# Kernel tuning notes

Measured on AMD Instinct MI355X. Metric: run time of the kernel, lower is better.

Reference implementation:

```python
import jax, jax.numpy as jnp
import numpy as np

D_MODEL = 2048
EXP_RATE = 4
DEPTH = 1
EPS = 1e-5

def setup_inputs() -> dict:
    key = jax.random.key(0)
    k1, k2 = jax.random.split(key, 2)
    B, T, D, E = 4, 4096, D_MODEL, EXP_RATE
    x = jax.random.normal(k1, (B, T, D), dtype=jnp.float32)
    residual = jax.random.normal(k2, (B, T, D), dtype=jnp.float32)
    # static_alpha = cat([alpha0, eye(E)], dim=1) -> [E, E+1]
    alpha0 = np.zeros((E, 1), dtype=np.float32)
    alpha0[DEPTH % E, 0] = 1.0
    static_alpha = jnp.asarray(np.concatenate([alpha0, np.eye(E, dtype=np.float32)], axis=1))
    static_beta = jnp.ones((E,), dtype=jnp.float32)
    dynamic_alpha_fn = jnp.zeros((D, E + 1), dtype=jnp.float32)
    dynamic_alpha_scale = jnp.ones((1,), dtype=jnp.float32) * 0.01
    dynamic_beta_fn = jnp.zeros((D,), dtype=jnp.float32)
    dynamic_beta_scale = jnp.ones((1,), dtype=jnp.float32) * 0.01
    rms_weight = jnp.ones((D,), dtype=jnp.float32)
    return {
        "x": x, "residual": residual, "rms_weight": rms_weight,
        "static_alpha": static_alpha, "static_beta": static_beta,
        "dynamic_alpha_fn": dynamic_alpha_fn, "dynamic_alpha_scale": dynamic_alpha_scale,
        "dynamic_beta_fn": dynamic_beta_fn, "dynamic_beta_scale": dynamic_beta_scale,
    }

def reference(x, residual, rms_weight, static_alpha, static_beta,
              dynamic_alpha_fn, dynamic_alpha_scale, dynamic_beta_fn, dynamic_beta_scale):
    # RMSNorm (elementwise affine)
    norm_x = x * jax.lax.rsqrt(jnp.mean(x * x, axis=-1, keepdims=True) + EPS) * rms_weight
    # Dynamic params
    dyn_alpha = jnp.tanh(norm_x @ dynamic_alpha_fn) * dynamic_alpha_scale  # [B,T,E+1]
    dyn_beta = jnp.tanh(norm_x @ dynamic_beta_fn) * dynamic_beta_scale[0]  # [B,T]
    alpha = static_alpha[None, None] + dyn_alpha[:, :, None, :]  # [B,T,E,E+1]
    beta = static_beta[None, None] + dyn_beta[:, :, None]        # [B,T,E]
    # Width connection: einsum('btij,btjd->btid', alpha^T, x_expanded) with
    # x_expanded[b,t,j,:] == x[b,t,:] for all j  =>  mix_h[b,t,i,:] = (sum_j alpha[b,t,j,i]) * x[b,t,:]
    coeff = alpha.sum(axis=2)  # [B,T,E+1]
    # Depth connection: sum_e beta_e * residual + sum_{i>=1} mix_h_i  (dropout = identity at eval)
    out = residual * beta.sum(axis=-1, keepdims=True) + x * coeff[..., 1:].sum(axis=-1, keepdims=True)
    return out
```

## Files before the change

### kernel.cpp

```cpp
#include <hip/hip_runtime.h>


#define D_MODEL 2048
#define E_RATE 4
#define HC_EPS 1e-5f
#define NT 256
#define EPT 8
#define TPB 8

__device__ __forceinline__ float fast_tanh(float z) {
    const float e = __builtin_amdgcn_exp2f(z * 2.8853900817779268f);
    return fmaf(-2.0f, __builtin_amdgcn_rcpf(e + 1.0f), 1.0f);
}

extern "C" __global__ void __launch_bounds__(NT, 4)
hc_kernel(const float* __restrict__ x,
          const float* __restrict__ resid,
          const float* __restrict__ w,
          const float* __restrict__ sA,
          const float* __restrict__ sB,
          const float* __restrict__ fnA,
          const float* __restrict__ aScale,
          const float* __restrict__ fnB,
          const float* __restrict__ bScale,
          float* __restrict__ out,
          const int n_tokens)
{
    const int tid  = threadIdx.x;
    const int tok0 = blockIdx.x * TPB;
    const int ntok = min(TPB, n_tokens - tok0);
    const int wave = tid >> 6, lane = tid & 63;

    float4 w0 = ((const float4*)w)[2 * tid];
    float4 w1 = ((const float4*)w)[2 * tid + 1];
    float4 b0 = ((const float4*)fnB)[2 * tid];
    float4 b1 = ((const float4*)fnB)[2 * tid + 1];

    float wf[EPT]  = {w0.x, w0.y, w0.z, w0.w, w1.x, w1.y, w1.z, w1.w};
    float fbf[EPT] = {b0.x, b0.y, b0.z, b0.w, b1.x, b1.y, b1.z, b1.w};

    float wb[EPT];
#pragma unroll
    for (int d = 0; d < EPT; d++) wb[d] = wf[d] * fbf[d];

    float wa[EPT][E_RATE];
    const float4* fa4 = (const float4*)fnA;
#pragma unroll
    for (int j = 0; j < 10; j++) {
        float4 t4 = fa4[(size_t)tid * 10 + j];
        float fv[4] = {t4.x, t4.y, t4.z, t4.w};
#pragma unroll
        for (int q = 0; q < 4; q++) {
            const int e = j * 4 + q;
            const int d = e / 5;
            const int i = e % 5;
            if (i >= 1) wa[d][i - 1] = fv[q] * wf[d];
        }
    }

    const float SB = sB[0] + sB[1] + sB[2] + sB[3];
    float SA = 0.0f;
#pragma unroll
    for (int i = 1; i <= E_RATE; i++)
#pragma unroll
        for (int j = 0; j < E_RATE; j++) SA += sA[j * (E_RATE + 1) + i];
    const float asc = aScale[0];
    const float bsc = bScale[0];

    __shared__ float red[2][4][8];

    const int F4 = D_MODEL / 4;
    const float4* xr   = (const float4*)(x     + (size_t)tok0 * D_MODEL);
    const float4* rr   = (const float4*)(resid + (size_t)tok0 * D_MODEL);
    float4*       orow = (float4*)(out + (size_t)tok0 * D_MODEL);

    float4 xn0 = xr[2 * tid], xn1 = xr[2 * tid + 1];
    float4 rn0 = rr[2 * tid], rn1 = rr[2 * tid + 1];

    for (int t = 0; t < ntok; ++t) {
        const float4 x0 = xn0, x1 = xn1, r0 = rn0, r1 = rn1;
        if (t + 1 < ntok) {
            const int nb = (t + 1) * F4 + 2 * tid;
            xn0 = xr[nb]; xn1 = xr[nb + 1];
            rn0 = rr[nb]; rn1 = rr[nb + 1];
        }

        const float xf[EPT] = {x0.x, x0.y, x0.z, x0.w, x1.x, x1.y, x1.z, x1.w};

        float vals[6] = {0.f, 0.f, 0.f, 0.f, 0.f, 0.f};
#pragma unroll
        for (int d = 0; d < EPT; d++) {
            vals[5] = fmaf(xf[d], xf[d], vals[5]);
            vals[4] = fmaf(xf[d], wb[d], vals[4]);
            vals[0] = fmaf(xf[d], wa[d][0], vals[0]);
            vals[1] = fmaf(xf[d], wa[d][1], vals[1]);
            vals[2] = fmaf(xf[d], wa[d][2], vals[2]);
            vals[3] = fmaf(xf[d], wa[d][3], vals[3]);
        }

#pragma unroll
        for (int j = 0; j < 6; j++) {
            float v = vals[j];
#pragma unroll
            for (int off = 32; off > 0; off >>= 1) v += __shfl_xor(v, off, 64);
            vals[j] = v;
        }

        const int p = t & 1;
        if (lane == 0) {
#pragma unroll
            for (int j = 0; j < 6; j++) red[p][wave][j] = vals[j];
        }
        asm volatile("s_waitcnt lgkmcnt(0)" ::: "memory");
        __builtin_amdgcn_s_barrier();
        asm volatile("" ::: "memory");

        float tot[6];
#pragma unroll
        for (int j = 0; j < 6; j++)
            tot[j] = (red[p][0][j] + red[p][1][j]) + (red[p][2][j] + red[p][3][j]);

        const float inv  = rsqrtf(tot[5] * (1.0f / D_MODEL) + HC_EPS);
        const float dynb = fast_tanh(tot[4] * inv) * bsc;
        float dyna = 0.0f;
#pragma unroll
        for (int i = 0; i < E_RATE; i++) dyna += fast_tanh(tot[i] * inv);

        const float cR = SB + (float)E_RATE * dynb;
        const float cX = SA + (float)E_RATE * (dyna * asc);

        float4 o0, o1;
        o0.x = fmaf(r0.x, cR, x0.x * cX);
        o0.y = fmaf(r0.y, cR, x0.y * cX);
        o0.z = fmaf(r0.z, cR, x0.z * cX);
        o0.w = fmaf(r0.w, cR, x0.w * cX);
        o1.x = fmaf(r1.x, cR, x1.x * cX);
        o1.y = fmaf(r1.y, cR, x1.y * cX);
        o1.z = fmaf(r1.z, cR, x1.z * cX);
        o1.w = fmaf(r1.w, cR, x1.w * cX);

        const int ob = t * F4 + 2 * tid;
        orow[ob]     = o0;
        orow[ob + 1] = o1;
    }
}

extern "C" void kernel_launch(void* const* d_in, const int* in_sizes, int n_in,
                              void* d_out, int out_size, void* d_ws, size_t ws_size,
                              hipStream_t stream) {
    const float* x      = (const float*)d_in[0];
    const float* resid  = (const float*)d_in[1];
    const float* w      = (const float*)d_in[2];
    const float* sA     = (const float*)d_in[3];
    const float* sB     = (const float*)d_in[4];
    const float* fnA    = (const float*)d_in[5];
    const float* aScale = (const float*)d_in[6];
    const float* fnB    = (const float*)d_in[7];
    const float* bScale = (const float*)d_in[8];
    float* out          = (float*)d_out;

    const int n_tokens = in_sizes[0] / D_MODEL;
    const int grid = (n_tokens + TPB - 1) / TPB;

    hc_kernel<<<grid, NT, 0, stream>>>(x, resid, w, sA, sB, fnA, aScale,
                                       fnB, bScale, out, n_tokens);
}
```

Measured before the change: 328.2 us.

## Assign one token row per wavefront with LDS-staged weight columns, drop block barriers

```diff
diff --git a/kernel.cpp b/kernel.cpp
--- a/kernel.cpp
+++ b/kernel.cpp
@@ -5,15 +5,16 @@
 #define E_RATE 4
 #define HC_EPS 1e-5f
 #define NT 256
-#define EPT 8
-#define TPB 8
+#define TPW 4
+#define F4ROW (D_MODEL / 4)
+#define CHUNKS 8
 
 __device__ __forceinline__ float fast_tanh(float z) {
     const float e = __builtin_amdgcn_exp2f(z * 2.8853900817779268f);
     return fmaf(-2.0f, __builtin_amdgcn_rcpf(e + 1.0f), 1.0f);
 }
 
-extern "C" __global__ void __launch_bounds__(NT, 4)
+extern "C" __global__ void __launch_bounds__(NT, 3)
 hc_kernel(const float* __restrict__ x,
           const float* __restrict__ resid,
           const float* __restrict__ w,
@@ -27,34 +28,44 @@
           const int n_tokens)
 {
     const int tid  = threadIdx.x;
-    const int tok0 = blockIdx.x * TPB;
-    const int ntok = min(TPB, n_tokens - tok0);
     const int wave = tid >> 6, lane = tid & 63;
 
-    float4 w0 = ((const float4*)w)[2 * tid];
-    float4 w1 = ((const float4*)w)[2 * tid + 1];
-    float4 b0 = ((const float4*)fnB)[2 * tid];
-    float4 b1 = ((const float4*)fnB)[2 * tid + 1];
+    __shared__ float4 wcol[5][512];
 
-    float wf[EPT]  = {w0.x, w0.y, w0.z, w0.w, w1.x, w1.y, w1.z, w1.w};
-    float fbf[EPT] = {b0.x, b0.y, b0.z, b0.w, b1.x, b1.y, b1.z, b1.w};
+    {
+        float4 w0 = ((const float4*)w)[2 * tid];
+        float4 w1 = ((const float4*)w)[2 * tid + 1];
+        float4 b0 = ((const float4*)fnB)[2 * tid];
+        float4 b1 = ((const float4*)fnB)[2 * tid + 1];
+        float wf[8]  = {w0.x, w0.y, w0.z, w0.w, w1.x, w1.y, w1.z, w1.w};
+        float fbf[8] = {b0.x, b0.y, b0.z, b0.w, b1.x, b1.y, b1.z, b1.w};
 
-    float wb[EPT];
+        float fa[40];
+        const float4* fa4 = (const float4*)fnA;
 #pragma unroll
-    for (int d = 0; d < EPT; d++) wb[d] = wf[d] * fbf[d];
-
-    float wa[EPT][E_RATE];
-    const float4* fa4 = (const float4*)fnA;
+        for (int j = 0; j < 10; j++) {
+            float4 t4 = fa4[(size_t)tid * 10 + j];
+            fa[4 * j + 0] = t4.x; fa[4 * j + 1] = t4.y;
+            fa[4 * j + 2] = t4.z; fa[4 * j + 3] = t4.w;
+        }
 #pragma unroll
-    for (int j = 0; j < 10; j++) {
-        float4 t4 = fa4[(size_t)tid * 10 + j];
-        float fv[4] = {t4.x, t4.y, t4.z, t4.w};
+        for (int lg = 0; lg < 2; lg++) {
+            const int g = tid * 2 + lg;
 #pragma unroll
-        for (int q = 0; q < 4; q++) {
-            const int e = j * 4 + q;
-            const int d = e / 5;
-            const int i = e % 5;
-            if (i >= 1) wa[d][i - 1] = fv[q] * wf[d];
+            for (int i = 0; i < 4; i++) {
+                float4 v;
+                v.x = fa[(4 * lg + 0) * 5 + i + 1] * wf[4 * lg + 0];
+                v.y = fa[(4 * lg + 1) * 5 + i + 1] * wf[4 * lg + 1];
+                v.z = fa[(4 * lg + 2) * 5 + i + 1] * wf[4 * lg + 2];
+                v.w = fa[(4 * lg + 3) * 5 + i + 1] * wf[4 * lg + 3];
+                wcol[i][g] = v;
+            }
+            float4 vb;
+            vb.x = fbf[4 * lg + 0] * wf[4 * lg + 0];
+            vb.y = fbf[4 * lg + 1] * wf[4 * lg + 1];
+            vb.z = fbf[4 * lg + 2] * wf[4 * lg + 2];
+            vb.w = fbf[4 * lg + 3] * wf[4 * lg + 3];
+            wcol[4][g] = vb;
         }
     }
 
@@ -67,37 +78,54 @@
     const float asc = aScale[0];
     const float bsc = bScale[0];
 
-    __shared__ float red[2][4][8];
+    __syncthreads();
 
-    const int F4 = D_MODEL / 4;
-    const float4* xr   = (const float4*)(x     + (size_t)tok0 * D_MODEL);
-    const float4* rr   = (const float4*)(resid + (size_t)tok0 * D_MODEL);
-    float4*       orow = (float4*)(out + (size_t)tok0 * D_MODEL);
+    const int gw   = blockIdx.x * (NT / 64) + wave;
+    const int tok0 = gw * TPW;
+    const int ntok = min(TPW, n_tokens - tok0);
+    if (ntok <= 0) return;
 
-    float4 xn0 = xr[2 * tid], xn1 = xr[2 * tid + 1];
-    float4 rn0 = rr[2 * tid], rn1 = rr[2 * tid + 1];
+    const float4* x4 = (const float4*)x;
+    const float4* r4 = (const float4*)resid;
+    float4*       o4 = (float4*)out;
+
+    float4 xa[CHUNKS], xb[CHUNKS], ra[CHUNKS];
+
+    {
+        const size_t b0 = (size_t)tok0 * F4ROW + lane;
+#pragma unroll
+        for (int c = 0; c < CHUNKS; c++) xa[c] = x4[b0 + c * 64];
+    }
 
     for (int t = 0; t < ntok; ++t) {
-        const float4 x0 = xn0, x1 = xn1, r0 = rn0, r1 = rn1;
+        const size_t rb = (size_t)(tok0 + t) * F4ROW + lane;
+
+#pragma unroll
+        for (int c = 0; c < CHUNKS; c++) ra[c] = r4[rb + c * 64];
         if (t + 1 < ntok) {
-            const int nb = (t + 1) * F4 + 2 * tid;
-            xn0 = xr[nb]; xn1 = xr[nb + 1];
-            rn0 = rr[nb]; rn1 = rr[nb + 1];
+#pragma unroll
+            for (int c = 0; c < CHUNKS; c++) xb[c] = x4[rb + F4ROW + c * 64];
         }
 
-        const float xf[EPT] = {x0.x, x0.y, x0.z, x0.w, x1.x, x1.y, x1.z, x1.w};
-
-        float vals[6] = {0.f, 0.f, 0.f, 0.f, 0.f, 0.f};
+        float a0 = 0.f, a1 = 0.f, a2 = 0.f, a3 = 0.f, ab = 0.f, ss = 0.f;
 #pragma unroll
-        for (int d = 0; d < EPT; d++) {
-            vals[5] = fmaf(xf[d], xf[d], vals[5]);
-            vals[4] = fmaf(xf[d], wb[d], vals[4]);
-            vals[0] = fmaf(xf[d], wa[d][0], vals[0]);
-            vals[1] = fmaf(xf[d], wa[d][1], vals[1]);
-            vals[2] = fmaf(xf[d], wa[d][2], vals[2]);
-            vals[3] = fmaf(xf[d], wa[d][3], vals[3]);
+        for (int c = 0; c < CHUNKS; c++) {
+            const int g = c * 64 + lane;
+            const float4 xv  = xa[c];
+            const float4 wv0 = wcol[0][g];
+            const float4 wv1 = wcol[1][g];
+            const float4 wv2 = wcol[2][g];
+            const float4 wv3 = wcol[3][g];
+            const float4 wvb = wcol[4][g];
+            ss = fmaf(xv.x, xv.x,  fmaf(xv.y, xv.y,  fmaf(xv.z, xv.z,  fmaf(xv.w, xv.w,  ss))));
+            a0 = fmaf(xv.x, wv0.x, fmaf(xv.y, wv0.y, fmaf(xv.z, wv0.z, fmaf(xv.w, wv0.w, a0))));
+            a1 = fmaf(xv.x, wv1.x, fmaf(xv.y, wv1.y, fmaf(xv.z, wv1.z, fmaf(xv.w, wv1.w, a1))));
+            a2 = fmaf(xv.x, wv2.x, fmaf(xv.y, wv2.y, fmaf(xv.z, wv2.z, fmaf(xv.w, wv2.w, a2))));
+            a3 = fmaf(xv.x, wv3.x, fmaf(xv.y, wv3.y, fmaf(xv.z, wv3.z, fmaf(xv.w, wv3.w, a3))));
+            ab = fmaf(xv.x, wvb.x, fmaf(xv.y, wvb.y, fmaf(xv.z, wvb.z, fmaf(xv.w, wvb.w, ab))));
         }
 
+        float vals[6] = {a0, a1, a2, a3, ab, ss};
 #pragma unroll
         for (int j = 0; j < 6; j++) {
             float v = vals[j];
@@ -106,42 +134,25 @@
             vals[j] = v;
         }
 
-        const int p = t & 1;
-        if (lane == 0) {
-#pragma unroll
-            for (int j = 0; j < 6; j++) red[p][wave][j] = vals[j];
-        }
-        asm volatile("s_waitcnt lgkmcnt(0)" ::: "memory");
-        __builtin_amdgcn_s_barrier();
-        asm volatile("" ::: "memory");
-
-        float tot[6];
-#pragma unroll
-        for (int j = 0; j < 6; j++)
-            tot[j] = (red[p][0][j] + red[p][1][j]) + (red[p][2][j] + red[p][3][j]);
-
-        const float inv  = rsqrtf(tot[5] * (1.0f / D_MODEL) + HC_EPS);
-        const float dynb = fast_tanh(tot[4] * inv) * bsc;
-        float dyna = 0.0f;
-#pragma unroll
-        for (int i = 0; i < E_RATE; i++) dyna += fast_tanh(tot[i] * inv);
-
+        const float inv  = rsqrtf(vals[5] * (1.0f / D_MODEL) + HC_EPS);
+        const float dynb = fast_tanh(vals[4] * inv) * bsc;
+        const float dyna = fast_tanh(vals[0] * inv) + fast_tanh(vals[1] * inv) +
+                           fast_tanh(vals[2] * inv) + fast_tanh(vals[3] * inv);
         const float cR = SB + (float)E_RATE * dynb;
         const float cX = SA + (float)E_RATE * (dyna * asc);
 
-        float4 o0, o1;
-        o0.x = fmaf(r0.x, cR, x0.x * cX);
-        o0.y = fmaf(r0.y, cR, x0.y * cX);
-        o0.z = fmaf(r0.z, cR, x0.z * cX);
-        o0.w = fmaf(r0.w, cR, x0.w * cX);
-        o1.x = fmaf(r1.x, cR, x1.x * cX);
-        o1.y = fmaf(r1.y, cR, x1.y * cX);
-        o1.z = fmaf(r1.z, cR, x1.z * cX);
-        o1.w = fmaf(r1.w, cR, x1.w * cX);
+#pragma unroll
+        for (int c = 0; c < CHUNKS; c++) {
+            float4 o;
+            o.x = fmaf(ra[c].x, cR, xa[c].x * cX);
+            o.y = fmaf(ra[c].y, cR, xa[c].y * cX);
+            o.z = fmaf(ra[c].z, cR, xa[c].z * cX);
+            o.w = fmaf(ra[c].w, cR, xa[c].w * cX);
+            o4[rb + c * 64] = o;
+        }
 
-        const int ob = t * F4 + 2 * tid;
-        orow[ob]     = o0;
-        orow[ob + 1] = o1;
+#pragma unroll
+        for (int c = 0; c < CHUNKS; c++) xa[c] = xb[c];
     }
 }
 
@@ -160,7 +171,8 @@
     float* out          = (float*)d_out;
 
     const int n_tokens = in_sizes[0] / D_MODEL;
-    const int grid = (n_tokens + TPB - 1) / TPB;
+    const int tok_per_block = (NT / 64) * TPW;
+    const int grid = (n_tokens + tok_per_block - 1) / tok_per_block;
 
     hc_kernel<<<grid, NT, 0, stream>>>(x, resid, w, sA, sB, fnA, aScale,
                                        fnB, bScale, out, n_tokens);
```

Result: slower. 481.7 us (+46.8%).
